# Kernel tuning notes

Measured on AMD Instinct MI355X. Metric: run time of the kernel, lower is better.

Reference implementation:

```python
import jax, jax.numpy as jnp
import numpy as np

EPS = 1e-5

def l2norm(x, axis=-1):
    # matches torch F.normalize(p=2): denom clamped at 1e-12
    n = jnp.linalg.norm(x, axis=axis, keepdims=True)
    return x / jnp.maximum(n, 1e-12)

def setup_inputs() -> dict:
    key = jax.random.key(0)
    ks = jax.random.split(key, 10)
    B, N, D, P = 8, 1024, 128, 16
    context = jax.random.normal(ks[0], (B, N, D), jnp.float32)
    acc_u = jax.random.normal(ks[1], (B, N, 1), jnp.float32)
    acc_v = jax.random.normal(ks[2], (B, N, 1), jnp.float32)
    uv_angle = jax.random.normal(ks[3], (B, N, 1), jnp.float32)
    uv_angleACC = jax.random.normal(ks[4], (B, N, 1), jnp.float32)
    speed = jax.random.normal(ks[5], (B, N, 1), jnp.float32)
    dist = jax.random.uniform(ks[6], (N, N), jnp.float32)
    angle = jax.random.normal(ks[7], (N, N), jnp.float32)
    # xavier_uniform for weight_tensor [P, D]: bound = sqrt(6/(P+D))
    bound = float(np.sqrt(6.0 / (P + D)))
    weight_tensor = jax.random.uniform(ks[8], (P, D), jnp.float32, -bound, bound)
    return {"context": context, "acc_u": acc_u, "acc_v": acc_v,
            "uv_angle": uv_angle, "uv_angleACC": uv_angleACC, "speed": speed,
            "isPhy": 1, "dist": dist, "angle": angle,
            "weight_tensor": weight_tensor}

def reference(context, acc_u, acc_v, uv_angle, uv_angleACC, speed, isPhy, dist, angle, weight_tensor):
    gamma, theta, sigma = 1.4, 0.5, 0.5
    P = weight_tensor.shape[0]
    N = context.shape[1]
    # --- weighted-cosine multi-perspective attention ---
    w = weight_tensor[:, None, None, :]                 # [P,1,1,D]
    context_fc = context[None] * w                      # [P,B,N,D]
    context_norm = l2norm(context_fc)                   # [P,B,N,D]
    # matmul over perspectives then mean over P
    attention = jnp.einsum('pbnd,pbmd->bnm', context_norm, context_norm) / P
    # --- epsilon neighbourhood (epsilon=0, markoff=0), mask detached ---
    mask = jax.lax.stop_gradient((attention > 0.0).astype(attention.dtype))
    attention = attention * mask
    # --- wind dynamics (pred_var 'u', isPhy True, dist given) ---
    Acc = acc_u * acc_u + acc_v * acc_v                 # [B,N,1]
    x1 = jnp.sqrt(Acc[:, :, 0] + EPS)                   # [B,N]
    x2 = jnp.abs(jnp.cos(uv_angleACC[:, :, 0] - uv_angle[:, :, 0]))
    temp_acc = x1 * x2                                  # [B,N]
    acc_part = temp_acc[:, :, None] * jnp.eye(N, dtype=attention.dtype)  # diag [B,N,N]
    spd = jax.lax.stop_gradient(speed)                  # speed.detach()
    ang = jax.lax.stop_gradient(angle)[None]            # torch.tensor() detaches
    d = jax.lax.stop_gradient(dist)[None] + EPS
    # uv_angle/speed broadcast [B,N,1] -> [B,N,N] (repeat along last dim)
    selfwind = jnp.abs(spd) * jnp.abs(jnp.cos(ang - uv_angle) + sigma * acc_part) / d
    selfwind = l2norm(selfwind)                         # [B,N,N]
    y = gamma * jnp.einsum('bnk,bmk->bnm', selfwind, selfwind) / 20.0 + EPS
    y = l2norm(y)
    u = l2norm(jnp.abs(theta * selfwind + jnp.sqrt(y)) + EPS)
    return attention * u
```

## Files before the change

kernel.cpp:

```cpp
#include <hip/hip_runtime.h>
#include <hip/hip_bf16.h>
#include <math.h>

#define EPSV 1e-5f

typedef __attribute__((ext_vector_type(4))) float f32x4;
typedef __attribute__((ext_vector_type(8))) short bf16x8;
typedef __attribute__((ext_vector_type(4))) unsigned short u16x4;

__device__ __forceinline__ unsigned short f2b(float x) {
  union { float f; unsigned int u; } v; v.f = x;
  unsigned int r = v.u + 0x7FFFu + ((v.u >> 16) & 1u);
  return (unsigned short)(r >> 16);
}
__device__ __forceinline__ float b2f(unsigned short h) {
  union { float f; unsigned int u; } v; v.u = ((unsigned int)h) << 16;
  return v.f;
}

__device__ __forceinline__ float block_reduce_sum(float v, float* sbuf) {
  #pragma unroll
  for (int off = 32; off; off >>= 1) v += __shfl_xor(v, off);
  __syncthreads();
  if ((threadIdx.x & 63) == 0) sbuf[threadIdx.x >> 6] = v;
  __syncthreads();
  return sbuf[0] + sbuf[1] + sbuf[2] + sbuf[3];
}

__global__ __launch_bounds__(256) void prep(const float* __restrict__ ctx,
                                            const float* __restrict__ wt,
                                            const float* __restrict__ speed,
                                            const float* __restrict__ uva,
                                            const float* __restrict__ accu,
                                            const float* __restrict__ accv,
                                            const float* __restrict__ uvaACC,
                                            const float* __restrict__ angle,
                                            const float* __restrict__ dist,
                                            unsigned short* __restrict__ V,
                                            unsigned short* __restrict__ SW,
                                            int BN, int N) {
  __shared__ float sbuf[4];
  const int blk = blockIdx.x;
  if (blk < BN) {
    const int bn = blk;
    const int w = threadIdx.x >> 6;
    const int lane = threadIdx.x & 63;
    const int p = w * 4 + (lane >> 4);
    const int dl = (lane & 15) * 8;
    const float* c = ctx + (size_t)bn * 128;
    const f32x4 ca = *(const f32x4*)(c + dl);
    const f32x4 cb = *(const f32x4*)(c + dl + 4);
    const f32x4 wa = *(const f32x4*)(wt + p * 128 + dl);
    const f32x4 wb = *(const f32x4*)(wt + p * 128 + dl + 4);
    float a[8];
    float ss = 0.0f;
    #pragma unroll
    for (int i = 0; i < 4; ++i) {
      a[i] = ca[i] * wa[i];
      a[4 + i] = cb[i] * wb[i];
      ss += a[i] * a[i] + a[4 + i] * a[4 + i];
    }
    ss += __shfl_xor(ss, 1);
    ss += __shfl_xor(ss, 2);
    ss += __shfl_xor(ss, 4);
    ss += __shfl_xor(ss, 8);
    const float inv = 1.0f / fmaxf(sqrtf(ss), 1e-12f);
    bf16x8 o;
    #pragma unroll
    for (int i = 0; i < 8; ++i) o[i] = (short)f2b(a[i] * inv);
    *(bf16x8*)(V + (size_t)bn * 2048 + p * 128 + dl) = o;
  } else {
    const int bn = blk - BN;
    const int n = bn & (N - 1);
    const int t = threadIdx.x;
    const float ua = uva[bn];
    const float sp = fabsf(speed[bn]);
    const float au = accu[bn], av = accv[bn];
    const float ta = sqrtf(au * au + av * av + EPSV) * fabsf(cosf(uvaACC[bn] - ua));
    const f32x4 an = *(const f32x4*)(angle + (size_t)n * N + 4 * t);
    const f32x4 dv = *(const f32x4*)(dist + (size_t)n * N + 4 * t);
    float v[4];
    float ss = 0.0f;
    #pragma unroll
    for (int i = 0; i < 4; ++i) {
      float cv = cosf(an[i] - ua);
      if (4 * t + i == n) cv += 0.5f * ta;
      v[i] = sp * fabsf(cv) / (dv[i] + EPSV);
      ss += v[i] * v[i];
    }
    ss = block_reduce_sum(ss, sbuf);
    const float inv = 1.0f / fmaxf(sqrtf(ss), 1e-12f);
    u16x4 o;
    #pragma unroll
    for (int i = 0; i < 4; ++i) o[i] = f2b(v[i] * inv);
    *(u16x4*)(SW + (size_t)bn * N + 4 * t) = o;
  }
}

__global__ __launch_bounds__(256) void gemm_fused(const unsigned short* __restrict__ V,
                                                  const unsigned short* __restrict__ SW,
                                                  float* __restrict__ OUT,
                                                  float* __restrict__ Y,
                                                  int N, int zoff) {
  __shared__ __align__(16) unsigned short As[2][128 * 32];
  __shared__ __align__(16) unsigned short Bs[2][128 * 32];
  const int z = blockIdx.z + zoff;
  const bool att = z < 8;
  const int b = att ? z : z - 8;
  const int K = att ? 2048 : 1024;
  const float scale = att ? (1.0f / 16.0f) : (1.4f / 20.0f);
  const unsigned short* Ab = att ? (V + (size_t)b * N * 2048)
                                 : (SW + (size_t)b * N * N);
  float* Cb = att ? (OUT + (size_t)b * N * N) : (Y + (size_t)b * N * N);

  const int n0 = blockIdx.x * 128;
  const int m0 = blockIdx.y * 128;
  const int tid = threadIdx.x;
  const int lane = tid & 63;
  const int wid = tid >> 6;
  const int wm = (wid >> 1) * 64;
  const int wn = (wid & 1) * 64;

  auto stage = [&](int buf, int k0) {
    #pragma unroll
    for (int i = 0; i < 2; ++i) {
      const int idx = i * 256 + tid;
      const int row = idx >> 2;
      const int cq = ((idx & 3) ^ ((row >> 1) & 3)) * 8;
      __builtin_amdgcn_global_load_lds(
          (const __attribute__((address_space(1))) unsigned int*)(Ab + (size_t)(m0 + row) * K + k0 + cq),
          (__attribute__((address_space(3))) unsigned int*)(&As[buf][idx * 8]), 16, 0, 0);
      __builtin_amdgcn_global_load_lds(
          (const __attribute__((address_space(1))) unsigned int*)(Ab + (size_t)(n0 + row) * K + k0 + cq),
          (__attribute__((address_space(3))) unsigned int*)(&Bs[buf][idx * 8]), 16, 0, 0);
    }
  };

  f32x4 acc[4][4] = {};
  stage(0, 0);
  __syncthreads();

  const int nk = K >> 5;
  for (int t = 0; t < nk; ++t) {
    const int cur = t & 1;
    if (t + 1 < nk) stage(cur ^ 1, (t + 1) << 5);

    bf16x8 af[4], bfr[4];
    const int c0 = lane >> 4;
    #pragma unroll
    for (int i = 0; i < 4; ++i) {
      const int r = wm + i * 16 + (lane & 15);
      af[i] = *(const bf16x8*)(&As[cur][r * 32 + ((c0 ^ ((r >> 1) & 3)) << 3)]);
    }
    #pragma unroll
    for (int j = 0; j < 4; ++j) {
      const int r = wn + j * 16 + (lane & 15);
      bfr[j] = *(const bf16x8*)(&Bs[cur][r * 32 + ((c0 ^ ((r >> 1) & 3)) << 3)]);
    }
    #pragma unroll
    for (int i = 0; i < 4; ++i)
      #pragma unroll
      for (int j = 0; j < 4; ++j)
        acc[i][j] = __builtin_amdgcn_mfma_f32_16x16x32_bf16(af[i], bfr[j], acc[i][j], 0, 0, 0);

    __syncthreads();
  }

  #pragma unroll
  for (int i = 0; i < 4; ++i) {
    #pragma unroll
    for (int r = 0; r < 4; ++r) {
      const int row = m0 + wm + i * 16 + (lane >> 4) * 4 + r;
      #pragma unroll
      for (int j = 0; j < 4; ++j) {
        const int col = n0 + wn + j * 16 + (lane & 15);
        float v = acc[i][j][r] * scale;
        v = att ? fmaxf(v, 0.0f) : (v + EPSV);
        Cb[(size_t)row * N + col] = v;
      }
    }
  }
}

__global__ __launch_bounds__(256) void finkern(const float* __restrict__ Y,
                                               const unsigned short* __restrict__ SW,
                                               float* __restrict__ OUT,
                                               int N) {
  __shared__ float sbuf[4];
  const int bn = blockIdx.x;
  const int t = threadIdx.x;
  const float* y = Y + (size_t)bn * N;
  const unsigned short* sw = SW + (size_t)bn * N;
  float* o = OUT + (size_t)bn * N;

  const f32x4 yv = *(const f32x4*)(y + 4 * t);
  float ss = yv[0] * yv[0] + yv[1] * yv[1] + yv[2] * yv[2] + yv[3] * yv[3];
  ss = block_reduce_sum(ss, sbuf);
  const float invy = 1.0f / fmaxf(sqrtf(ss), 1e-12f);

  const u16x4 swv = *(const u16x4*)(sw + 4 * t);
  float tv[4];
  float st = 0.0f;
  #pragma unroll
  for (int i = 0; i < 4; ++i) {
    tv[i] = fabsf(0.5f * b2f(swv[i]) + sqrtf(yv[i] * invy)) + EPSV;
    st += tv[i] * tv[i];
  }
  st = block_reduce_sum(st, sbuf);
  const float invt = 1.0f / fmaxf(sqrtf(st), 1e-12f);

  f32x4 ov = *(f32x4*)(o + 4 * t);
  #pragma unroll
  for (int i = 0; i < 4; ++i) ov[i] *= tv[i] * invt;
  *(f32x4*)(o + 4 * t) = ov;
}

extern "C" void kernel_launch(void* const* d_in, const int* in_sizes, int n_in,
                              void* d_out, int out_size, void* d_ws, size_t ws_size,
                              hipStream_t stream) {
  const float* ctx        = (const float*)d_in[0];
  const float* acc_u      = (const float*)d_in[1];
  const float* acc_v      = (const float*)d_in[2];
  const float* uv_angle   = (const float*)d_in[3];
  const float* uv_angleACC= (const float*)d_in[4];
  const float* speed      = (const float*)d_in[5];
  const float* dist       = (const float*)d_in[7];
  const float* angle      = (const float*)d_in[8];
  const float* wt         = (const float*)d_in[9];

  const int B = 8, N = 1024, P = 16, D = 128;
  const int K1 = P * D;
  const int BN = B * N;

  const size_t szV  = (size_t)BN * K1 * 2;
  const size_t szSW = (size_t)BN * N * 2;
  const size_t szY  = (size_t)BN * N * 4;

  unsigned short* V  = (unsigned short*)d_ws;
  unsigned short* SW = (unsigned short*)((char*)d_ws + szV);
  float* out = (float*)d_out;

  prep<<<dim3(2 * BN), dim3(256), 0, stream>>>(ctx, wt, speed, uv_angle, acc_u,
                                               acc_v, uv_angleACC, angle, dist,
                                               V, SW, BN, N);

  if (ws_size >= szV + szSW + szY) {
    float* Yp = (float*)((char*)d_ws + szV + szSW);
    gemm_fused<<<dim3(N / 128, N / 128, 16), dim3(256), 0, stream>>>(V, SW, out, Yp, N, 0);
    finkern<<<dim3(BN), dim3(256), 0, stream>>>(Yp, SW, out, N);
  } else {
    float* Yp = (float*)d_ws;
    gemm_fused<<<dim3(N / 128, N / 128, 8), dim3(256), 0, stream>>>(V, SW, out, Yp, N, 0);
    gemm_fused<<<dim3(N / 128, N / 128, 8), dim3(256), 0, stream>>>(V, SW, out, Yp, N, 8);
    finkern<<<dim3(BN), dim3(256), 0, stream>>>(Yp, SW, out, N);
  }
}
```

Measured before the change: 194.3 us.

## Rewrite batched GEMM as 256x256-tile 8-wave kernel with ping-pong pipelining

Replaces the 128x128-tile, 4-wave GEMM with a 256x256-tile, 512-thread kernel. It uses explicit s_waitcnt and barrier scheduling to interleave global-to-LDS staging with MFMA quads, raises MFMA priority with setprio, and flattens the grid to a 1D launch with batch-interleaved block mapping. The goal is more operand reuse per LDS load and better overlap of loads with MFMA work, cutting global traffic and stalls. The cost is more registers (256 launch-bound occupancy at 2 blocks) and only 256 blocks on the device, which risks underfilling the CUs.

```diff
diff --git a/kernel.cpp b/kernel.cpp
--- a/kernel.cpp
+++ b/kernel.cpp
@@ -3,6 +3,8 @@
 #include <math.h>
 
 #define EPSV 1e-5f
+#define AS1 __attribute__((address_space(1)))
+#define AS3 __attribute__((address_space(3)))
 
 typedef __attribute__((ext_vector_type(4))) float f32x4;
 typedef __attribute__((ext_vector_type(8))) short bf16x8;
@@ -97,86 +99,125 @@
   }
 }
 
-__global__ __launch_bounds__(256) void gemm_fused(const unsigned short* __restrict__ V,
-                                                  const unsigned short* __restrict__ SW,
-                                                  float* __restrict__ OUT,
-                                                  float* __restrict__ Y,
-                                                  int N, int zoff) {
-  __shared__ __align__(16) unsigned short As[2][128 * 32];
-  __shared__ __align__(16) unsigned short Bs[2][128 * 32];
-  const int z = blockIdx.z + zoff;
+#define FENCE asm volatile("" ::: "memory")
+__device__ __forceinline__ void barx() { FENCE; __builtin_amdgcn_s_barrier(); FENCE; }
+
+#define QUAD(QI)                                                                 \
+  { _Pragma("unroll") for (int i2 = 0; i2 < 4; ++i2) {                           \
+      _Pragma("unroll") for (int j = 0; j < 4; ++j)                              \
+        acc[(QI)*4 + i2][j] = __builtin_amdgcn_mfma_f32_16x16x32_bf16(           \
+            af[i2], bf[j], acc[(QI)*4 + i2][j], 0, 0, 0); } }
+
+__global__ __launch_bounds__(512, 2) void gemm8(const unsigned short* __restrict__ V,
+                                                const unsigned short* __restrict__ SW,
+                                                float* __restrict__ OUT,
+                                                float* __restrict__ Y,
+                                                int zmask, int zshift, int zoff) {
+  __shared__ __align__(16) unsigned short As[2][256 * 32];
+  __shared__ __align__(16) unsigned short Bs[2][256 * 32];
+  const int bid = blockIdx.x;
+  const int z = (bid & zmask) + zoff;
+  const int tix = bid >> zshift;
+  const int n0 = (tix & 3) * 256;
+  const int m0 = (tix >> 2) * 256;
   const bool att = z < 8;
   const int b = att ? z : z - 8;
   const int K = att ? 2048 : 1024;
+  const int NN = 1024;
   const float scale = att ? (1.0f / 16.0f) : (1.4f / 20.0f);
-  const unsigned short* Ab = att ? (V + (size_t)b * N * 2048)
-                                 : (SW + (size_t)b * N * N);
-  float* Cb = att ? (OUT + (size_t)b * N * N) : (Y + (size_t)b * N * N);
-
-  const int n0 = blockIdx.x * 128;
-  const int m0 = blockIdx.y * 128;
+  const unsigned short* Ab = att ? (V + (size_t)b * NN * 2048) : (SW + (size_t)b * NN * NN);
+  float* Cb = att ? (OUT + (size_t)b * NN * NN) : (Y + (size_t)b * NN * NN);
+
   const int tid = threadIdx.x;
   const int lane = tid & 63;
   const int wid = tid >> 6;
-  const int wm = (wid >> 1) * 64;
-  const int wn = (wid & 1) * 64;
-
-  auto stage = [&](int buf, int k0) {
-    #pragma unroll
-    for (int i = 0; i < 2; ++i) {
-      const int idx = i * 256 + tid;
+  const int wm = (wid >> 2) * 128;
+  const int wn = (wid & 3) * 64;
+  const int fr = lane & 15;
+  const int fc = lane >> 4;
+
+  f32x4 acc[8][4] = {};
+  bf16x8 af[4], bf[4];
+
+  auto stage = [&](unsigned short* dstbuf, int rbase, int kt) {
+    const int k0 = kt << 5;
+    #pragma unroll
+    for (int e = 0; e < 2; ++e) {
+      const int idx = e * 512 + tid;
       const int row = idx >> 2;
-      const int cq = ((idx & 3) ^ ((row >> 1) & 3)) * 8;
+      const int pc = idx & 3;
+      const int c = pc ^ ((row >> 1) & 3);
       __builtin_amdgcn_global_load_lds(
-          (const __attribute__((address_space(1))) unsigned int*)(Ab + (size_t)(m0 + row) * K + k0 + cq),
-          (__attribute__((address_space(3))) unsigned int*)(&As[buf][idx * 8]), 16, 0, 0);
-      __builtin_amdgcn_global_load_lds(
-          (const __attribute__((address_space(1))) unsigned int*)(Ab + (size_t)(n0 + row) * K + k0 + cq),
-          (__attribute__((address_space(3))) unsigned int*)(&Bs[buf][idx * 8]), 16, 0, 0);
+          (const AS1 unsigned int*)(Ab + (size_t)(rbase + row) * K + k0 + (c << 3)),
+          (AS3 unsigned int*)(dstbuf + idx * 8), 16, 0, 0);
     }
   };
-
-  f32x4 acc[4][4] = {};
-  stage(0, 0);
-  __syncthreads();
+  auto lda4 = [&](const unsigned short* buf, int ib) {
+    #pragma unroll
+    for (int i2 = 0; i2 < 4; ++i2) {
+      const int r = wm + (ib + i2) * 16 + fr;
+      af[i2] = *(const bf16x8*)(buf + r * 32 + ((fc ^ ((r >> 1) & 3)) << 3));
+    }
+  };
+  auto ldb4 = [&](const unsigned short* buf) {
+    #pragma unroll
+    for (int j = 0; j < 4; ++j) {
+      const int r = wn + j * 16 + fr;
+      bf[j] = *(const bf16x8*)(buf + r * 32 + ((fc ^ ((r >> 1) & 3)) << 3));
+    }
+  };
 
   const int nk = K >> 5;
-  for (int t = 0; t < nk; ++t) {
-    const int cur = t & 1;
-    if (t + 1 < nk) stage(cur ^ 1, (t + 1) << 5);
-
-    bf16x8 af[4], bfr[4];
-    const int c0 = lane >> 4;
-    #pragma unroll
-    for (int i = 0; i < 4; ++i) {
-      const int r = wm + i * 16 + (lane & 15);
-      af[i] = *(const bf16x8*)(&As[cur][r * 32 + ((c0 ^ ((r >> 1) & 3)) << 3)]);
-    }
-    #pragma unroll
-    for (int j = 0; j < 4; ++j) {
-      const int r = wn + j * 16 + (lane & 15);
-      bfr[j] = *(const bf16x8*)(&Bs[cur][r * 32 + ((c0 ^ ((r >> 1) & 3)) << 3)]);
-    }
-    #pragma unroll
-    for (int i = 0; i < 4; ++i)
-      #pragma unroll
-      for (int j = 0; j < 4; ++j)
-        acc[i][j] = __builtin_amdgcn_mfma_f32_16x16x32_bf16(af[i], bfr[j], acc[i][j], 0, 0, 0);
-
-    __syncthreads();
-  }
-
-  #pragma unroll
-  for (int i = 0; i < 4; ++i) {
+  const int niter = nk >> 1;
+
+  stage(Bs[0], n0, 0);
+  stage(As[0], m0, 0);
+  stage(Bs[1], n0, 1);
+  asm volatile("s_waitcnt vmcnt(2)" ::: "memory");
+  barx();
+
+  for (int k = 0; k < niter; ++k) {
+    const int t0 = 2 * k, t1 = t0 + 1;
+    lda4(As[0], 0); ldb4(Bs[0]);
+    stage(As[1], m0, t1);
+    barx();
+    __builtin_amdgcn_s_setprio(1); QUAD(0); __builtin_amdgcn_s_setprio(0);
+    asm volatile("s_waitcnt lgkmcnt(0)" ::: "memory");
+    barx();
+    lda4(As[0], 4);
+    if (t0 + 2 < nk) stage(Bs[0], n0, t0 + 2);
+    barx();
+    __builtin_amdgcn_s_setprio(1); QUAD(1); __builtin_amdgcn_s_setprio(0);
+    asm volatile("s_waitcnt lgkmcnt(0)" ::: "memory");
+    if (k + 1 < niter) { asm volatile("s_waitcnt vmcnt(2)" ::: "memory"); }
+    else               { asm volatile("s_waitcnt vmcnt(0)" ::: "memory"); }
+    barx();
+    lda4(As[1], 0); ldb4(Bs[1]);
+    if (t0 + 2 < nk) stage(As[0], m0, t0 + 2);
+    barx();
+    __builtin_amdgcn_s_setprio(1); QUAD(0); __builtin_amdgcn_s_setprio(0);
+    asm volatile("s_waitcnt lgkmcnt(0)" ::: "memory");
+    barx();
+    lda4(As[1], 4);
+    if (t1 + 2 < nk) stage(Bs[1], n0, t1 + 2);
+    barx();
+    __builtin_amdgcn_s_setprio(1); QUAD(1); __builtin_amdgcn_s_setprio(0);
+    asm volatile("s_waitcnt lgkmcnt(0)" ::: "memory");
+    asm volatile("s_waitcnt vmcnt(2)" ::: "memory");
+    barx();
+  }
+
+  #pragma unroll
+  for (int i = 0; i < 8; ++i) {
     #pragma unroll
     for (int r = 0; r < 4; ++r) {
-      const int row = m0 + wm + i * 16 + (lane >> 4) * 4 + r;
+      const int row = m0 + wm + i * 16 + fc * 4 + r;
       #pragma unroll
       for (int j = 0; j < 4; ++j) {
-        const int col = n0 + wn + j * 16 + (lane & 15);
+        const int col = n0 + wn + j * 16 + fr;
         float v = acc[i][j][r] * scale;
         v = att ? fmaxf(v, 0.0f) : (v + EPSV);
-        Cb[(size_t)row * N + col] = v;
+        Cb[(size_t)row * NN + col] = v;
       }
     }
   }
@@ -228,8 +269,8 @@
   const float* angle      = (const float*)d_in[8];
   const float* wt         = (const float*)d_in[9];
 
-  const int B = 8, N = 1024, P = 16, D = 128;
-  const int K1 = P * D;
+  const int B = 8, N = 1024, P = 16;
+  const int K1 = P * 128;
   const int BN = B * N;
 
   const size_t szV  = (size_t)BN * K1 * 2;
@@ -246,12 +287,12 @@
 
   if (ws_size >= szV + szSW + szY) {
     float* Yp = (float*)((char*)d_ws + szV + szSW);
-    gemm_fused<<<dim3(N / 128, N / 128, 16), dim3(256), 0, stream>>>(V, SW, out, Yp, N, 0);
+    gemm8<<<dim3(256), dim3(512), 0, stream>>>(V, SW, out, Yp, 15, 4, 0);
     finkern<<<dim3(BN), dim3(256), 0, stream>>>(Yp, SW, out, N);
   } else {
     float* Yp = (float*)d_ws;
-    gemm_fused<<<dim3(N / 128, N / 128, 8), dim3(256), 0, stream>>>(V, SW, out, Yp, N, 0);
-    gemm_fused<<<dim3(N / 128, N / 128, 8), dim3(256), 0, stream>>>(V, SW, out, Yp, N, 8);
+    gemm8<<<dim3(128), dim3(512), 0, stream>>>(V, SW, out, Yp, 7, 3, 0);
+    gemm8<<<dim3(128), dim3(512), 0, stream>>>(V, SW, out, Yp, 7, 3, 8);
     finkern<<<dim3(BN), dim3(256), 0, stream>>>(Yp, SW, out, N);
   }
 }
```

Measured after the change: 187.1 us. -3.7%, faster.

## Rewrite batched GEMM with 128x256 tiles, triple-buffered LDS, and bf16 Y

Applied to the files above, without the earlier changes.

The fused GEMM now uses 512-thread blocks computing 128x256 output tiles, with a three-stage LDS ring buffer. Manual vmcnt waits and raw barriers keep two global-to-LDS loads in flight while the MFMA loop raises its wave priority. The Y intermediate is stored as bf16 instead of fp32, halving its write and read traffic in the final normalization kernel. Block ordering interleaves batches within the attention and wind halves. This trades some precision in Y and more LDS per block for more data reuse and better load/compute overlap.

```diff
diff --git a/kernel.cpp b/kernel.cpp
--- a/kernel.cpp
+++ b/kernel.cpp
@@ -3,6 +3,8 @@
 #include <math.h>
 
 #define EPSV 1e-5f
+#define AS1 __attribute__((address_space(1)))
+#define AS3 __attribute__((address_space(3)))
 
 typedef __attribute__((ext_vector_type(4))) float f32x4;
 typedef __attribute__((ext_vector_type(8))) short bf16x8;
@@ -97,104 +99,144 @@
   }
 }
 
-__global__ __launch_bounds__(256) void gemm_fused(const unsigned short* __restrict__ V,
-                                                  const unsigned short* __restrict__ SW,
-                                                  float* __restrict__ OUT,
-                                                  float* __restrict__ Y,
-                                                  int N, int zoff) {
-  __shared__ __align__(16) unsigned short As[2][128 * 32];
-  __shared__ __align__(16) unsigned short Bs[2][128 * 32];
-  const int z = blockIdx.z + zoff;
-  const bool att = z < 8;
-  const int b = att ? z : z - 8;
+#define FENCE asm volatile("" ::: "memory")
+__device__ __forceinline__ void barx() { FENCE; __builtin_amdgcn_s_barrier(); FENCE; }
+
+__global__ __launch_bounds__(512, 4) void gemm8(const unsigned short* __restrict__ V,
+                                                const unsigned short* __restrict__ SW,
+                                                float* __restrict__ OUT,
+                                                unsigned short* __restrict__ Yb,
+                                                int boff) {
+  __shared__ __align__(16) unsigned short As[3][128 * 32];
+  __shared__ __align__(16) unsigned short Bs[3][256 * 32];
+  const int id = blockIdx.x + boff;
+  const bool att = id < 256;
+  const int r = att ? id : id - 256;
+  const int b = r & 7;
+  const int tile = r >> 3;
+  const int m0 = (tile & 7) * 128;
+  const int n0 = (tile >> 3) * 256;
   const int K = att ? 2048 : 1024;
-  const float scale = att ? (1.0f / 16.0f) : (1.4f / 20.0f);
-  const unsigned short* Ab = att ? (V + (size_t)b * N * 2048)
-                                 : (SW + (size_t)b * N * N);
-  float* Cb = att ? (OUT + (size_t)b * N * N) : (Y + (size_t)b * N * N);
-
-  const int n0 = blockIdx.x * 128;
-  const int m0 = blockIdx.y * 128;
+  const int NN = 1024;
+  const unsigned short* Ab = att ? (V + (size_t)b * NN * 2048) : (SW + (size_t)b * NN * NN);
+
   const int tid = threadIdx.x;
   const int lane = tid & 63;
   const int wid = tid >> 6;
-  const int wm = (wid >> 1) * 64;
-  const int wn = (wid & 1) * 64;
-
-  auto stage = [&](int buf, int k0) {
-    #pragma unroll
-    for (int i = 0; i < 2; ++i) {
-      const int idx = i * 256 + tid;
+  const int wm = (wid >> 2) * 64;
+  const int wn = (wid & 3) * 64;
+  const int fr = lane & 15;
+  const int fc = lane >> 4;
+  const int rsw = (fc ^ ((fr >> 1) & 3)) << 3;
+
+  f32x4 acc[4][4] = {};
+  bf16x8 af[4], bf[4];
+
+  auto stage = [&](int sb, int kt) {
+    const int k0 = kt << 5;
+    {
+      const int row = tid >> 2;
+      const int c = (tid & 3) ^ ((row >> 1) & 3);
+      __builtin_amdgcn_global_load_lds(
+          (const AS1 unsigned int*)(Ab + (size_t)(m0 + row) * K + k0 + (c << 3)),
+          (AS3 unsigned int*)(&As[sb][tid * 8]), 16, 0, 0);
+    }
+    #pragma unroll
+    for (int e = 0; e < 2; ++e) {
+      const int idx = e * 512 + tid;
       const int row = idx >> 2;
-      const int cq = ((idx & 3) ^ ((row >> 1) & 3)) * 8;
+      const int c = (idx & 3) ^ ((row >> 1) & 3);
       __builtin_amdgcn_global_load_lds(
-          (const __attribute__((address_space(1))) unsigned int*)(Ab + (size_t)(m0 + row) * K + k0 + cq),
-          (__attribute__((address_space(3))) unsigned int*)(&As[buf][idx * 8]), 16, 0, 0);
-      __builtin_amdgcn_global_load_lds(
-          (const __attribute__((address_space(1))) unsigned int*)(Ab + (size_t)(n0 + row) * K + k0 + cq),
-          (__attribute__((address_space(3))) unsigned int*)(&Bs[buf][idx * 8]), 16, 0, 0);
+          (const AS1 unsigned int*)(Ab + (size_t)(n0 + row) * K + k0 + (c << 3)),
+          (AS3 unsigned int*)(&Bs[sb][idx * 8]), 16, 0, 0);
     }
   };
 
-  f32x4 acc[4][4] = {};
+  const int nk = K >> 5;
+
   stage(0, 0);
-  __syncthreads();
-
-  const int nk = K >> 5;
+  stage(1, 1);
+  asm volatile("s_waitcnt vmcnt(3)" ::: "memory");
+  barx();
+
+  int rd = 0;
   for (int t = 0; t < nk; ++t) {
-    const int cur = t & 1;
-    if (t + 1 < nk) stage(cur ^ 1, (t + 1) << 5);
-
-    bf16x8 af[4], bfr[4];
-    const int c0 = lane >> 4;
-    #pragma unroll
-    for (int i = 0; i < 4; ++i) {
-      const int r = wm + i * 16 + (lane & 15);
-      af[i] = *(const bf16x8*)(&As[cur][r * 32 + ((c0 ^ ((r >> 1) & 3)) << 3)]);
-    }
-    #pragma unroll
-    for (int j = 0; j < 4; ++j) {
-      const int r = wn + j * 16 + (lane & 15);
-      bfr[j] = *(const bf16x8*)(&Bs[cur][r * 32 + ((c0 ^ ((r >> 1) & 3)) << 3)]);
-    }
+    const unsigned short* Ar = As[rd];
+    const unsigned short* Br = Bs[rd];
+    #pragma unroll
+    for (int i = 0; i < 4; ++i)
+      af[i] = *(const bf16x8*)(Ar + (wm + i * 16 + fr) * 32 + rsw);
+    #pragma unroll
+    for (int j = 0; j < 4; ++j)
+      bf[j] = *(const bf16x8*)(Br + (wn + j * 16 + fr) * 32 + rsw);
+
+    if (t + 2 < nk) {
+      int st = rd + 2; if (st >= 3) st -= 3;
+      stage(st, t + 2);
+    }
+    barx();
+    asm volatile("s_waitcnt lgkmcnt(0)" ::: "memory");
+    __builtin_amdgcn_s_setprio(1);
     #pragma unroll
     for (int i = 0; i < 4; ++i)
       #pragma unroll
       for (int j = 0; j < 4; ++j)
-        acc[i][j] = __builtin_amdgcn_mfma_f32_16x16x32_bf16(af[i], bfr[j], acc[i][j], 0, 0, 0);
-
-    __syncthreads();
-  }
-
-  #pragma unroll
-  for (int i = 0; i < 4; ++i) {
-    #pragma unroll
-    for (int r = 0; r < 4; ++r) {
-      const int row = m0 + wm + i * 16 + (lane >> 4) * 4 + r;
+        acc[i][j] = __builtin_amdgcn_mfma_f32_16x16x32_bf16(af[i], bf[j], acc[i][j], 0, 0, 0);
+    __builtin_amdgcn_s_setprio(0);
+    if (t + 2 < nk)      { asm volatile("s_waitcnt vmcnt(3)" ::: "memory"); }
+    else if (t + 1 < nk) { asm volatile("s_waitcnt vmcnt(0)" ::: "memory"); }
+    barx();
+    rd = (rd + 1 == 3) ? 0 : rd + 1;
+  }
+
+  if (att) {
+    float* Cb = OUT + (size_t)b * NN * NN;
+    #pragma unroll
+    for (int i = 0; i < 4; ++i)
       #pragma unroll
-      for (int j = 0; j < 4; ++j) {
-        const int col = n0 + wn + j * 16 + (lane & 15);
-        float v = acc[i][j][r] * scale;
-        v = att ? fmaxf(v, 0.0f) : (v + EPSV);
-        Cb[(size_t)row * N + col] = v;
+      for (int rr = 0; rr < 4; ++rr) {
+        const int row = m0 + wm + i * 16 + fc * 4 + rr;
+        #pragma unroll
+        for (int j = 0; j < 4; ++j) {
+          const int col = n0 + wn + j * 16 + fr;
+          Cb[(size_t)row * NN + col] = fmaxf(acc[i][j][rr] * (1.0f / 16.0f), 0.0f);
+        }
       }
-    }
-  }
-}
-
-__global__ __launch_bounds__(256) void finkern(const float* __restrict__ Y,
+  } else {
+    unsigned short* Cb = Yb + (size_t)b * NN * NN;
+    #pragma unroll
+    for (int i = 0; i < 4; ++i)
+      #pragma unroll
+      for (int rr = 0; rr < 4; ++rr) {
+        const int row = m0 + wm + i * 16 + fc * 4 + rr;
+        #pragma unroll
+        for (int j = 0; j < 4; ++j) {
+          const int col = n0 + wn + j * 16 + fr;
+          Cb[(size_t)row * NN + col] = f2b(acc[i][j][rr] * (1.4f / 20.0f) + EPSV);
+        }
+      }
+  }
+}
+
+__global__ __launch_bounds__(256) void finkern(const unsigned short* __restrict__ Yb,
                                                const unsigned short* __restrict__ SW,
                                                float* __restrict__ OUT,
                                                int N) {
   __shared__ float sbuf[4];
   const int bn = blockIdx.x;
   const int t = threadIdx.x;
-  const float* y = Y + (size_t)bn * N;
+  const unsigned short* y = Yb + (size_t)bn * N;
   const unsigned short* sw = SW + (size_t)bn * N;
   float* o = OUT + (size_t)bn * N;
 
-  const f32x4 yv = *(const f32x4*)(y + 4 * t);
-  float ss = yv[0] * yv[0] + yv[1] * yv[1] + yv[2] * yv[2] + yv[3] * yv[3];
+  const u16x4 yraw = *(const u16x4*)(y + 4 * t);
+  float yv[4];
+  float ss = 0.0f;
+  #pragma unroll
+  for (int i = 0; i < 4; ++i) {
+    yv[i] = b2f(yraw[i]);
+    ss += yv[i] * yv[i];
+  }
   ss = block_reduce_sum(ss, sbuf);
   const float invy = 1.0f / fmaxf(sqrtf(ss), 1e-12f);
 
@@ -228,13 +270,13 @@
   const float* angle      = (const float*)d_in[8];
   const float* wt         = (const float*)d_in[9];
 
-  const int B = 8, N = 1024, P = 16, D = 128;
-  const int K1 = P * D;
+  const int B = 8, N = 1024, P = 16;
+  const int K1 = P * 128;
   const int BN = B * N;
 
   const size_t szV  = (size_t)BN * K1 * 2;
   const size_t szSW = (size_t)BN * N * 2;
-  const size_t szY  = (size_t)BN * N * 4;
+  const size_t szYb = (size_t)BN * N * 2;
 
   unsigned short* V  = (unsigned short*)d_ws;
   unsigned short* SW = (unsigned short*)((char*)d_ws + szV);
@@ -244,14 +286,14 @@
                                                acc_v, uv_angleACC, angle, dist,
                                                V, SW, BN, N);
 
-  if (ws_size >= szV + szSW + szY) {
-    float* Yp = (float*)((char*)d_ws + szV + szSW);
-    gemm_fused<<<dim3(N / 128, N / 128, 16), dim3(256), 0, stream>>>(V, SW, out, Yp, N, 0);
+  if (ws_size >= szV + szSW + szYb) {
+    unsigned short* Yp = (unsigned short*)((char*)d_ws + szV + szSW);
+    gemm8<<<dim3(512), dim3(512), 0, stream>>>(V, SW, out, Yp, 0);
     finkern<<<dim3(BN), dim3(256), 0, stream>>>(Yp, SW, out, N);
   } else {
-    float* Yp = (float*)d_ws;
-    gemm_fused<<<dim3(N / 128, N / 128, 8), dim3(256), 0, stream>>>(V, SW, out, Yp, N, 0);
-    gemm_fused<<<dim3(N / 128, N / 128, 8), dim3(256), 0, stream>>>(V, SW, out, Yp, N, 8);
+    unsigned short* Yp = (unsigned short*)d_ws;
+    gemm8<<<dim3(256), dim3(512), 0, stream>>>(V, SW, out, Yp, 0);
+    gemm8<<<dim3(256), dim3(512), 0, stream>>>(V, SW, out, Yp, 256);
     finkern<<<dim3(BN), dim3(256), 0, stream>>>(Yp, SW, out, N);
   }
 }
```

Result: faster. 172.0 us (-11.5%).
